# Kernel optimization log

Hardware: AMD Instinct MI355X
Metric: run time of the kernel (lower is better)

The kernel has to match this reference:

```python
import jax, jax.numpy as jnp
import numpy as np

H = 256      # hidden_dim
NH = 4       # num_heads (fixed in __init__)


def _mha_pool(x, mask, Wqkv, bqkv, Wo, bo):
    """Batched torch-style MultiheadAttention (self-attn) + masked mean pool.
    x: [..., L, H], mask: [..., L] float {0,1} (1 = valid).
    Returns pooled embedding [..., H]. Fully-masked rows yield zeros
    (numerator is 0, denominator is 1e-10), matching the torch branch.
    """
    h = x.shape[-1]
    dh = h // NH
    qkv = x @ Wqkv.T + bqkv                      # [..., L, 3H]
    q, k, v = jnp.split(qkv, 3, axis=-1)
    split = lambda t: t.reshape(t.shape[:-1] + (NH, dh))
    q, k, v = split(q), split(k), split(v)
    scale = 1.0 / jnp.sqrt(jnp.asarray(dh, x.dtype))
    scores = jnp.einsum('...qhd,...khd->...hqk', q, k) * scale
    # key_padding_mask: masked keys get large negative logit
    scores = scores + (1.0 - mask)[..., None, None, :] * jnp.asarray(-1e9, x.dtype)
    attn = jax.nn.softmax(scores, axis=-1)
    o = jnp.einsum('...hqk,...khd->...qhd', attn, v)
    o = o.reshape(o.shape[:-2] + (h,)) @ Wo.T + bo   # out_proj
    pooled = (o * mask[..., None]).sum(-2) / (mask.sum(-1, keepdims=True) + 1e-10)
    return pooled


def _mha_params(key):
    k1, k2 = jax.random.split(key)
    s = 1.0 / np.sqrt(H)
    Wqkv = jax.random.uniform(k1, (3 * H, H), jnp.float32, -s, s)
    bqkv = jnp.zeros((3 * H,), jnp.float32)
    Wo = jax.random.uniform(k2, (H, H), jnp.float32, -s, s)
    bo = jnp.zeros((H,), jnp.float32)
    return Wqkv, bqkv, Wo, bo


def setup_inputs() -> dict:
    key = jax.random.key(0)
    k0, k1, kw, ks, kc = jax.random.split(key, 5)
    B, SEC, SEN, W = 16, 8, 16, 64
    we = jax.random.normal(k0, (B, SEC, SEN, W, H), jnp.float32)
    am = jax.random.randint(k1, (B, SEC, SEN, W), 0, 2, jnp.int32)
    wW, wb, wO, wob = _mha_params(kw)
    sW, sb, sO, sob = _mha_params(ks)
    cW, cb, cO, cob = _mha_params(kc)
    return {
        'word_embeddings': we, 'attention_mask': am,
        'word_Wqkv': wW, 'word_bqkv': wb, 'word_Wo': wO, 'word_bo': wob,
        'sent_Wqkv': sW, 'sent_bqkv': sb, 'sent_Wo': sO, 'sent_bo': sob,
        'sect_Wqkv': cW, 'sect_bqkv': cb, 'sect_Wo': cO, 'sect_bo': cob,
    }


def reference(word_embeddings, attention_mask,
              word_Wqkv, word_bqkv, word_Wo, word_bo,
              sent_Wqkv, sent_bqkv, sent_Wo, sent_bo,
              sect_Wqkv, sect_bqkv, sect_Wo, sect_bo):
    wm = attention_mask.astype(word_embeddings.dtype)            # [B,Sec,Sen,W]
    # word level -> sentence embeddings [B,Sec,Sen,H]
    sent = _mha_pool(word_embeddings, wm, word_Wqkv, word_bqkv, word_Wo, word_bo)
    # sentence level -> section embeddings [B,Sec,H]
    sm = (wm.sum(-1) > 0).astype(word_embeddings.dtype)          # [B,Sec,Sen]
    sect = _mha_pool(sent, sm, sent_Wqkv, sent_bqkv, sent_Wo, sent_bo)
    # section level -> doc embeddings [B,H]
    cm = (wm.sum((-1, -2)) > 0).astype(word_embeddings.dtype)    # [B,Sec]
    doc = _mha_pool(sect, cm, sect_Wqkv, sect_bqkv, sect_Wo, sect_bo)
    return doc
```

## Files before the change

### kernel.cpp

```cpp
#include <hip/hip_runtime.h>
#include <hip/hip_bf16.h>


typedef short bf16x8 __attribute__((ext_vector_type(8)));
typedef float f32x4 __attribute__((ext_vector_type(4)));
typedef unsigned int u32x4 __attribute__((ext_vector_type(4)));
typedef unsigned short U16;
typedef unsigned int U32;

__device__ __forceinline__ U32 bf16_rne(float f) {
    U32 u = __builtin_bit_cast(U32, f);
    return (u + 0x7FFFu + ((u >> 16) & 1u)) >> 16;
}
__device__ __forceinline__ void split_hl(float f, U16& h, U16& l) {
    U32 hu = bf16_rne(f);
    float hf = __builtin_bit_cast(float, hu << 16);
    h = (U16)hu;
    l = (U16)bf16_rne(f - hf);
}
__device__ __forceinline__ U32 pack_hl(float f) {
    U32 hu = bf16_rne(f);
    float hf = __builtin_bit_cast(float, hu << 16);
    U32 lo = bf16_rne(f - hf);
    return (hu << 16) | (lo & 0xFFFFu);
}

__device__ __forceinline__ void unpack8(u32x4 a, u32x4 b, u32x4& hi, u32x4& lo) {
    hi[0] = __builtin_amdgcn_perm(a[1], a[0], 0x07060302u);
    hi[1] = __builtin_amdgcn_perm(a[3], a[2], 0x07060302u);
    hi[2] = __builtin_amdgcn_perm(b[1], b[0], 0x07060302u);
    hi[3] = __builtin_amdgcn_perm(b[3], b[2], 0x07060302u);
    lo[0] = __builtin_amdgcn_perm(a[1], a[0], 0x05040100u);
    lo[1] = __builtin_amdgcn_perm(a[3], a[2], 0x05040100u);
    lo[2] = __builtin_amdgcn_perm(b[1], b[0], 0x05040100u);
    lo[3] = __builtin_amdgcn_perm(b[3], b[2], 0x05040100u);
}

#define MFMA(A, B, C) __builtin_amdgcn_mfma_f32_16x16x32_bf16( \
    __builtin_bit_cast(bf16x8, A), __builtin_bit_cast(bf16x8, B), C, 0, 0, 0)

__device__ __forceinline__ void tile_frag(const U32* tile, int row, int s0,
                                          u32x4& hi, u32x4& lo) {
    int m = row & 15;
    u32x4 a = *(const u32x4*)(tile + row * 64 + ((s0    ) ^ m) * 4);
    u32x4 b = *(const u32x4*)(tile + row * 64 + ((s0 + 1) ^ m) * 4);
    unpack8(a, b, hi, lo);
}
__device__ __forceinline__ void tile_put(U32* tile, int row, int col, float v) {
    tile[row * 64 + (((col >> 2) ^ (row & 15))) * 4 + (col & 3)] = pack_hl(v);
}

template <int RS, int SW>
__device__ __forceinline__ u32x4 fragp(const U16* base, int row, int k, int lhi) {
    int slot = ((k >> 3) + lhi) ^ (row & SW);
    return *(const u32x4*)(base + row * RS + slot * 8);
}
template <int RS, int SW>
__device__ __forceinline__ void put16(U16* base, int row, int col, U16 v) {
    int slot = (col >> 3) ^ (row & SW);
    base[row * RS + slot * 8 + (col & 7)] = v;
}
template <int RS, int SW>
__device__ __forceinline__ void put64(U16* base, int row, int col0,
                                      U16 v0, U16 v1, U16 v2, U16 v3) {
    int slot = (col0 >> 3) ^ (row & SW);
    U32* p = (U32*)(base + row * RS + slot * 8 + (col0 & 7));
    p[0] = (U32)v0 | ((U32)v1 << 16);
    p[1] = (U32)v2 | ((U32)v3 << 16);
}

__global__ __launch_bounds__(256) void convert_w(
    const float* __restrict__ Wq, const float* __restrict__ Wo,
    U16* __restrict__ qh, U16* __restrict__ ql,
    U16* __restrict__ oh, U16* __restrict__ ol)
{
    int i = blockIdx.x * 256 + threadIdx.x;
    if (i < 768 * 256) { U16 h, l; split_hl(Wq[i], h, l); qh[i] = h; ql[i] = l; }
    if (i < 256 * 256) { U16 h, l; split_hl(Wo[i], h, l); oh[i] = h; ol[i] = l; }
}

__global__ __launch_bounds__(256, 2) void word_mfma(
    const float* __restrict__ x, const int* __restrict__ am,
    const U16* __restrict__ Wqh, const U16* __restrict__ Wql,
    const float* __restrict__ bqkv,
    const float* __restrict__ Wo32,
    const float* __restrict__ bo,
    U16* __restrict__ sent_hi, U16* __restrict__ sent_lo,
    float* __restrict__ smask)
{
    __shared__ __align__(16) U32 Qs[64 * 64];
    __shared__ __align__(16) U32 Ks[64 * 64];
    __shared__ __align__(16) U32 VX[64 * 64];
    __shared__ float msk[64];
    __shared__ float smsum;

    const int t = threadIdx.x;
    const int w = t >> 6, l = t & 63, l15 = l & 15, lhi = l >> 4;
    const int b = blockIdx.x;
    const float* xb = x + (size_t)b * 16384;

    if (t < 64) msk[t] = (float)am[b * 64 + t];

    const int r0 = t >> 3, c8 = t & 7;
    const int r1 = r0 + 32;
    const int mm0 = r0 & 15, mm1 = r1 & 15;

    float po[16];

    #pragma unroll 1
    for (int h = 0; h < 4; ++h) {
        float4 s00 = *(const float4*)(xb + r0 * 256 + c8 * 8);
        float4 s01 = *(const float4*)(xb + r0 * 256 + c8 * 8 + 4);
        float4 s10 = *(const float4*)(xb + r1 * 256 + c8 * 8);
        float4 s11 = *(const float4*)(xb + r1 * 256 + c8 * 8 + 4);
        f32x4 acc[3][4];
        #pragma unroll
        for (int j = 0; j < 3; ++j)
            #pragma unroll
            for (int mt = 0; mt < 4; ++mt) acc[j][mt] = f32x4{0.f, 0.f, 0.f, 0.f};

        for (int kc = 0; kc < 4; ++kc) {
            __syncthreads();
            {
                u32x4 p0, p1;
                p0[0] = pack_hl(s00.x); p0[1] = pack_hl(s00.y);
                p0[2] = pack_hl(s00.z); p0[3] = pack_hl(s00.w);
                p1[0] = pack_hl(s01.x); p1[1] = pack_hl(s01.y);
                p1[2] = pack_hl(s01.z); p1[3] = pack_hl(s01.w);
                *(u32x4*)(VX + r0 * 64 + ((c8 * 2    ) ^ mm0) * 4) = p0;
                *(u32x4*)(VX + r0 * 64 + ((c8 * 2 + 1) ^ mm0) * 4) = p1;
                p0[0] = pack_hl(s10.x); p0[1] = pack_hl(s10.y);
                p0[2] = pack_hl(s10.z); p0[3] = pack_hl(s10.w);
                p1[0] = pack_hl(s11.x); p1[1] = pack_hl(s11.y);
                p1[2] = pack_hl(s11.z); p1[3] = pack_hl(s11.w);
                *(u32x4*)(VX + r1 * 64 + ((c8 * 2    ) ^ mm1) * 4) = p0;
                *(u32x4*)(VX + r1 * 64 + ((c8 * 2 + 1) ^ mm1) * 4) = p1;
            }
            __syncthreads();
            if (kc < 3) {
                s00 = *(const float4*)(xb + r0 * 256 + (kc + 1) * 64 + c8 * 8);
                s01 = *(const float4*)(xb + r0 * 256 + (kc + 1) * 64 + c8 * 8 + 4);
                s10 = *(const float4*)(xb + r1 * 256 + (kc + 1) * 64 + c8 * 8);
                s11 = *(const float4*)(xb + r1 * 256 + (kc + 1) * 64 + c8 * 8 + 4);
            }
            #pragma unroll
            for (int ks = 0; ks < 2; ++ks) {
                const int s0 = ks * 8 + lhi * 2;
                const int kk = kc * 64 + ks * 32 + lhi * 8;
                const size_t wr0 = (size_t)(          h * 64 + w * 16 + l15) * 256 + kk;
                const size_t wr1 = (size_t)(256     + h * 64 + w * 16 + l15) * 256 + kk;
                const size_t wr2 = (size_t)(512     + h * 64 + w * 16 + l15) * 256 + kk;
                u32x4 wh0 = *(const u32x4*)(Wqh + wr0);
                u32x4 wl0 = *(const u32x4*)(Wql + wr0);
                u32x4 wh1 = *(const u32x4*)(Wqh + wr1);
                u32x4 wl1 = *(const u32x4*)(Wql + wr1);
                u32x4 wh2 = *(const u32x4*)(Wqh + wr2);
                u32x4 wl2 = *(const u32x4*)(Wql + wr2);
                #pragma unroll
                for (int mt = 0; mt < 4; ++mt) {
                    u32x4 xh, xl;
                    tile_frag(VX, mt * 16 + l15, s0, xh, xl);
                    acc[0][mt] = MFMA(xh, wh0, acc[0][mt]);
                    acc[0][mt] = MFMA(xh, wl0, acc[0][mt]);
                    acc[0][mt] = MFMA(xl, wh0, acc[0][mt]);
                    acc[1][mt] = MFMA(xh, wh1, acc[1][mt]);
                    acc[1][mt] = MFMA(xh, wl1, acc[1][mt]);
                    acc[1][mt] = MFMA(xl, wh1, acc[1][mt]);
                    acc[2][mt] = MFMA(xh, wh2, acc[2][mt]);
                    acc[2][mt] = MFMA(xh, wl2, acc[2][mt]);
                    acc[2][mt] = MFMA(xl, wh2, acc[2][mt]);
                }
            }
        }
        {
            const float bQ = bqkv[      h * 64 + w * 16 + l15];
            const float bK = bqkv[256 + h * 64 + w * 16 + l15];
            #pragma unroll
            for (int mt = 0; mt < 4; ++mt) {
                #pragma unroll
                for (int r = 0; r < 4; ++r) {
                    tile_put(Qs, mt * 16 + lhi * 4 + r, w * 16 + l15, acc[0][mt][r] + bQ);
                    tile_put(Ks, mt * 16 + lhi * 4 + r, w * 16 + l15, acc[1][mt][r] + bK);
                }
            }
        }
        __syncthreads();
        {
            const float bV = bqkv[512 + h * 64 + w * 16 + l15];
            const int d = w * 16 + l15;
            #pragma unroll
            for (int mt = 0; mt < 4; ++mt) {
                u32x4 pv;
                #pragma unroll
                for (int r = 0; r < 4; ++r) pv[r] = pack_hl(acc[2][mt][r] + bV);
                const int cs = (mt * 4 + lhi) ^ (d & 15);
                *(u32x4*)(VX + d * 64 + cs * 4) = pv;
            }
        }
        __syncthreads();
        if (h == 0 && t == 0) {
            float s = 0.f;
            for (int i = 0; i < 64; ++i) s += msk[i];
            smsum = s;
        }

        {
            f32x4 sa[4];
            #pragma unroll
            for (int i = 0; i < 4; ++i) sa[i] = f32x4{0.f, 0.f, 0.f, 0.f};
            #pragma unroll
            for (int ks = 0; ks < 2; ++ks) {
                const int s0 = ks * 8 + lhi * 2;
                u32x4 qh, ql;
                tile_frag(Qs, w * 16 + l15, s0, qh, ql);
                #pragma unroll
                for (int nt = 0; nt < 4; ++nt) {
                    u32x4 kh, kl;
                    tile_frag(Ks, nt * 16 + l15, s0, kh, kl);
                    sa[nt] = MFMA(qh, kh, sa[nt]);
                    sa[nt] = MFMA(qh, kl, sa[nt]);
                    sa[nt] = MFMA(ql, kh, sa[nt]);
                }
            }
            float sc[4][4];
            #pragma unroll
            for (int nt = 0; nt < 4; ++nt) {
                const float mterm = (1.0f - msk[nt * 16 + l15]) * -1e9f;
                #pragma unroll
                for (int r = 0; r < 4; ++r) sc[nt][r] = sa[nt][r] * 0.125f + mterm;
            }
            #pragma unroll
            for (int r = 0; r < 4; ++r) {
                float m = fmaxf(fmaxf(sc[0][r], sc[1][r]), fmaxf(sc[2][r], sc[3][r]));
                #pragma unroll
                for (int off = 1; off < 16; off <<= 1) m = fmaxf(m, __shfl_xor(m, off));
                float e0 = expf(sc[0][r] - m), e1 = expf(sc[1][r] - m);
                float e2 = expf(sc[2][r] - m), e3 = expf(sc[3][r] - m);
                float s = e0 + e1 + e2 + e3;
                #pragma unroll
                for (int off = 1; off < 16; off <<= 1) s += __shfl_xor(s, off);
                const float inv = 1.0f / s;
                sc[0][r] = e0 * inv; sc[1][r] = e1 * inv;
                sc[2][r] = e2 * inv; sc[3][r] = e3 * inv;
            }
            #pragma unroll
            for (int nt = 0; nt < 4; ++nt)
                #pragma unroll
                for (int r = 0; r < 4; ++r)
                    tile_put(Qs, w * 16 + lhi * 4 + r, nt * 16 + l15, sc[nt][r]);
        }
        {
            f32x4 pa[4];
            #pragma unroll
            for (int i = 0; i < 4; ++i) pa[i] = f32x4{0.f, 0.f, 0.f, 0.f};
            #pragma unroll
            for (int ks = 0; ks < 2; ++ks) {
                const int s0 = ks * 8 + lhi * 2;
                u32x4 ph, pl;
                tile_frag(Qs, w * 16 + l15, s0, ph, pl);
                #pragma unroll
                for (int nt = 0; nt < 4; ++nt) {
                    u32x4 vh, vl;
                    tile_frag(VX, nt * 16 + l15, s0, vh, vl);
                    pa[nt] = MFMA(ph, vh, pa[nt]);
                    pa[nt] = MFMA(ph, vl, pa[nt]);
                    pa[nt] = MFMA(pl, vh, pa[nt]);
                }
            }
            float sarr[4];
            #pragma unroll
            for (int nt = 0; nt < 4; ++nt) {
                float s = 0.f;
                #pragma unroll
                for (int r = 0; r < 4; ++r)
                    s += msk[w * 16 + lhi * 4 + r] * pa[nt][r];
                s += __shfl_xor(s, 16);
                s += __shfl_xor(s, 32);
                sarr[nt] = s;
            }
            if (h == 0) {
                po[0] = sarr[0]; po[1] = sarr[1]; po[2] = sarr[2]; po[3] = sarr[3];
            } else if (h == 1) {
                po[4] = sarr[0]; po[5] = sarr[1]; po[6] = sarr[2]; po[7] = sarr[3];
            } else if (h == 2) {
                po[8] = sarr[0]; po[9] = sarr[1]; po[10] = sarr[2]; po[11] = sarr[3];
            } else {
                po[12] = sarr[0]; po[13] = sarr[1]; po[14] = sarr[2]; po[15] = sarr[3];
            }
        }
    }

    __syncthreads();
    float (*part)[256] = (float(*)[256])Ks;
    if (lhi == 0) {
        #pragma unroll
        for (int hh = 0; hh < 4; ++hh)
            #pragma unroll
            for (int nt = 0; nt < 4; ++nt)
                part[w][hh * 64 + nt * 16 + l15] = po[hh * 4 + nt];
    }
    __syncthreads();
    {
        float opv = part[0][t] + part[1][t] + part[2][t] + part[3][t];
        part[0][t] = opv;
    }
    __syncthreads();
    {
        const float* wrow = Wo32 + (size_t)t * 256;
        const float* opool = part[0];
        float s = 0.f;
        #pragma unroll 8
        for (int c = 0; c < 256; c += 4) {
            float4 wv = *(const float4*)(wrow + c);
            s += opool[c] * wv.x + opool[c + 1] * wv.y
               + opool[c + 2] * wv.z + opool[c + 3] * wv.w;
        }
        float m = smsum;
        float val = (s + bo[t] * m) / (m + 1e-10f);
        U16 vH, vL; split_hl(val, vH, vL);
        sent_hi[(size_t)b * 256 + t] = vH;
        sent_lo[(size_t)b * 256 + t] = vL;
    }
    if (t == 0) smask[b] = (smsum > 0.f) ? 1.f : 0.f;
}

template <int L>
__global__ __launch_bounds__(256) void mha_small(
    const U16* __restrict__ xh, const U16* __restrict__ xl,
    const float* __restrict__ mk,
    const U16* __restrict__ Wqh, const U16* __restrict__ Wql,
    const float* __restrict__ bqkv,
    const U16* __restrict__ Woh, const U16* __restrict__ Wol,
    const float* __restrict__ bo,
    float* __restrict__ out_f32, U16* __restrict__ out_hi, U16* __restrict__ out_lo,
    float* __restrict__ outmask)
{
    __shared__ __align__(16) U16 xs_h[16*256], xs_l[16*256];
    __shared__ __align__(16) U16 Qh_[16*256], Ql_[16*256];
    __shared__ __align__(16) U16 Kh_[16*256], Kl_[16*256];
    __shared__ __align__(16) U16 Vh_[256*32], Vl_[256*32];
    __shared__ __align__(16) U16 Ph_[4][16*32], Pl_[4][16*32];
    __shared__ __align__(16) U16 Oh_[16*256], Ol_[16*256];
    __shared__ float msk[16];
    __shared__ float smsum;

    const int t = threadIdx.x;
    const int w = t >> 6, l = t & 63, l15 = l & 15, lhi = l >> 4;
    const int b = blockIdx.x;

    if (t < 16) msk[t] = (t < L) ? mk[b*L + t] : 0.f;

    #pragma unroll
    for (int i = 0; i < 2; ++i) {
        int c = i*256 + t;
        int row = c >> 5, c8 = c & 31;
        u32x4 hv = u32x4{0,0,0,0}, lv = u32x4{0,0,0,0};
        if (row < L) {
            hv = *(const u32x4*)(xh + ((size_t)b*L + row)*256 + c8*8);
            lv = *(const u32x4*)(xl + ((size_t)b*L + row)*256 + c8*8);
        }
        int slot = c8 ^ (row & 7);
        *(u32x4*)(xs_h + row*256 + slot*8) = hv;
        *(u32x4*)(xs_l + row*256 + slot*8) = lv;
    }
    #pragma unroll
    for (int i = 0; i < 4; ++i) {
        int c = i*256 + t;
        *(u32x4*)(Vh_ + c*8) = u32x4{0,0,0,0};
        *(u32x4*)(Vl_ + c*8) = u32x4{0,0,0,0};
    }
    *(u32x4*)(&Ph_[0][0] + t*8) = u32x4{0,0,0,0};
    *(u32x4*)(&Pl_[0][0] + t*8) = u32x4{0,0,0,0};
    __syncthreads();
    if (t == 0) { float s = 0.f; for (int i = 0; i < 16; ++i) s += msk[i]; smsum = s; }

    {
        f32x4 acc[12];
        #pragma unroll
        for (int i = 0; i < 12; ++i) acc[i] = f32x4{0.f,0.f,0.f,0.f};
        #pragma unroll 2
        for (int k0 = 0; k0 < 256; k0 += 32) {
            u32x4 ah = fragp<256,7>(xs_h, l15, k0, lhi);
            u32x4 al = fragp<256,7>(xs_l, l15, k0, lhi);
            #pragma unroll
            for (int j = 0; j < 12; ++j) {
                int u = w*12 + j;
                u32x4 wh = *(const u32x4*)(Wqh + (size_t)(u*16 + l15)*256 + k0 + lhi*8);
                u32x4 wl = *(const u32x4*)(Wql + (size_t)(u*16 + l15)*256 + k0 + lhi*8);
                acc[j] = MFMA(ah, wh, acc[j]);
                acc[j] = MFMA(ah, wl, acc[j]);
                acc[j] = MFMA(al, wh, acc[j]);
            }
        }
        #pragma unroll
        for (int j = 0; j < 12; ++j) {
            int u = w*12 + j;
            int mat = u >> 4, cg = u & 15;
            float bias = bqkv[u*16 + l15];
            if (mat < 2) {
                U16* dh = (mat == 0) ? Qh_ : Kh_;
                U16* dl = (mat == 0) ? Ql_ : Kl_;
                #pragma unroll
                for (int r = 0; r < 4; ++r) {
                    U16 vH, vL; split_hl(acc[j][r] + bias, vH, vL);
                    put16<256,7>(dh, lhi*4 + r, cg*16 + l15, vH);
                    put16<256,7>(dl, lhi*4 + r, cg*16 + l15, vL);
                }
            } else {
                U16 h4[4], l4[4];
                #pragma unroll
                for (int r = 0; r < 4; ++r) split_hl(acc[j][r] + bias, h4[r], l4[r]);
                put64<32,3>(Vh_, cg*16 + l15, lhi*4, h4[0],h4[1],h4[2],h4[3]);
                put64<32,3>(Vl_, cg*16 + l15, lhi*4, l4[0],l4[1],l4[2],l4[3]);
            }
        }
    }
    __syncthreads();

    {
        const int h = w;
        f32x4 sa = f32x4{0.f,0.f,0.f,0.f};
        #pragma unroll
        for (int k0 = 0; k0 < 64; k0 += 32) {
            u32x4 qh = fragp<256,7>(Qh_, l15, h*64 + k0, lhi);
            u32x4 ql = fragp<256,7>(Ql_, l15, h*64 + k0, lhi);
            u32x4 kh = fragp<256,7>(Kh_, l15, h*64 + k0, lhi);
            u32x4 kl = fragp<256,7>(Kl_, l15, h*64 + k0, lhi);
            sa = MFMA(qh, kh, sa);
            sa = MFMA(qh, kl, sa);
            sa = MFMA(ql, kh, sa);
        }
        float sc[4];
        float mterm = (1.0f - msk[l15]) * -1e9f;
        #pragma unroll
        for (int r = 0; r < 4; ++r) sc[r] = sa[r] * 0.125f + mterm;
        #pragma unroll
        for (int r = 0; r < 4; ++r) {
            float m = sc[r];
            #pragma unroll
            for (int off = 1; off < 16; off <<= 1) m = fmaxf(m, __shfl_xor(m, off));
            float e = expf(sc[r] - m);
            float s = e;
            #pragma unroll
            for (int off = 1; off < 16; off <<= 1) s += __shfl_xor(s, off);
            sc[r] = e / s;
        }
        #pragma unroll
        for (int r = 0; r < 4; ++r) {
            U16 vH, vL; split_hl(sc[r], vH, vL);
            put16<32,3>(&Ph_[h][0], lhi*4 + r, l15, vH);
            put16<32,3>(&Pl_[h][0], lhi*4 + r, l15, vL);
        }
        f32x4 pa[4];
        #pragma unroll
        for (int i = 0; i < 4; ++i) pa[i] = f32x4{0.f,0.f,0.f,0.f};
        {
            u32x4 ph = fragp<32,3>(&Ph_[h][0], l15, 0, lhi);
            u32x4 pl = fragp<32,3>(&Pl_[h][0], l15, 0, lhi);
            #pragma unroll
            for (int ntl = 0; ntl < 4; ++ntl) {
                u32x4 vh = fragp<32,3>(Vh_, h*64 + ntl*16 + l15, 0, lhi);
                u32x4 vl = fragp<32,3>(Vl_, h*64 + ntl*16 + l15, 0, lhi);
                pa[ntl] = MFMA(ph, vh, pa[ntl]);
                pa[ntl] = MFMA(ph, vl, pa[ntl]);
                pa[ntl] = MFMA(pl, vh, pa[ntl]);
            }
        }
        #pragma unroll
        for (int ntl = 0; ntl < 4; ++ntl) {
            #pragma unroll
            for (int r = 0; r < 4; ++r) {
                U16 vH, vL; split_hl(pa[ntl][r], vH, vL);
                put16<256,7>(Oh_, lhi*4 + r, h*64 + ntl*16 + l15, vH);
                put16<256,7>(Ol_, lhi*4 + r, h*64 + ntl*16 + l15, vL);
            }
        }
    }
    __syncthreads();

    {
        f32x4 acc4[4];
        #pragma unroll
        for (int i = 0; i < 4; ++i) acc4[i] = f32x4{0.f,0.f,0.f,0.f};
        #pragma unroll 2
        for (int k0 = 0; k0 < 256; k0 += 32) {
            u32x4 oh = fragp<256,7>(Oh_, l15, k0, lhi);
            u32x4 ol = fragp<256,7>(Ol_, l15, k0, lhi);
            #pragma unroll
            for (int j = 0; j < 4; ++j) {
                int oc = w*64 + j*16 + l15;
                u32x4 wh = *(const u32x4*)(Woh + (size_t)oc*256 + k0 + lhi*8);
                u32x4 wl = *(const u32x4*)(Wol + (size_t)oc*256 + k0 + lhi*8);
                acc4[j] = MFMA(oh, wh, acc4[j]);
                acc4[j] = MFMA(oh, wl, acc4[j]);
                acc4[j] = MFMA(ol, wh, acc4[j]);
            }
        }
        float msum = smsum;
        #pragma unroll
        for (int j = 0; j < 4; ++j) {
            float s = 0.f;
            #pragma unroll
            for (int r = 0; r < 4; ++r) s += msk[lhi*4 + r] * acc4[j][r];
            s += __shfl_xor(s, 16);
            s += __shfl_xor(s, 32);
            if (lhi == 0) {
                int col = w*64 + j*16 + l15;
                float val = (s + bo[col] * msum) / (msum + 1e-10f);
                if (out_f32) out_f32[(size_t)b*256 + col] = val;
                if (out_hi) {
                    U16 vH, vL; split_hl(val, vH, vL);
                    out_hi[(size_t)b*256 + col] = vH;
                    out_lo[(size_t)b*256 + col] = vL;
                }
            }
        }
    }
    if (t == 0 && outmask) outmask[b] = (smsum > 0.f) ? 1.f : 0.f;
}

extern "C" void kernel_launch(void* const* d_in, const int* in_sizes, int n_in,
                              void* d_out, int out_size, void* d_ws, size_t ws_size,
                              hipStream_t stream) {
    (void)in_sizes; (void)n_in; (void)out_size; (void)ws_size;
    const float* we  = (const float*)d_in[0];
    const int*   am  = (const int*)d_in[1];
    const float* wW  = (const float*)d_in[2];
    const float* wb  = (const float*)d_in[3];
    const float* wO  = (const float*)d_in[4];
    const float* wob = (const float*)d_in[5];
    const float* sW  = (const float*)d_in[6];
    const float* sb  = (const float*)d_in[7];
    const float* sO  = (const float*)d_in[8];
    const float* sob = (const float*)d_in[9];
    const float* cW  = (const float*)d_in[10];
    const float* cb  = (const float*)d_in[11];
    const float* cO  = (const float*)d_in[12];
    const float* cob = (const float*)d_in[13];

    U16* p = (U16*)d_ws;
    U16* sent_hi = p; p += 2048*256;
    U16* sent_lo = p; p += 2048*256;
    U16* sect_hi = p; p += 128*256;
    U16* sect_lo = p; p += 128*256;
    U16* w1qh = p; p += 768*256;  U16* w1ql = p; p += 768*256;
    U16* w1oh = p; p += 256*256;  U16* w1ol = p; p += 256*256;
    U16* w2qh = p; p += 768*256;  U16* w2ql = p; p += 768*256;
    U16* w2oh = p; p += 256*256;  U16* w2ol = p; p += 256*256;
    U16* w3qh = p; p += 768*256;  U16* w3ql = p; p += 768*256;
    U16* w3oh = p; p += 256*256;  U16* w3ol = p; p += 256*256;
    float* smaskb = (float*)p;
    float* cmaskb = smaskb + 2048;

    convert_w<<<768, 256, 0, stream>>>(wW, wO, w1qh, w1ql, w1oh, w1ol);
    convert_w<<<768, 256, 0, stream>>>(sW, sO, w2qh, w2ql, w2oh, w2ol);
    convert_w<<<768, 256, 0, stream>>>(cW, cO, w3qh, w3ql, w3oh, w3ol);
    word_mfma<<<2048, 256, 0, stream>>>(we, am, w1qh, w1ql, wb, wO, wob,
                                        sent_hi, sent_lo, smaskb);
    mha_small<16><<<128, 256, 0, stream>>>(sent_hi, sent_lo, smaskb,
                                           w2qh, w2ql, sb, w2oh, w2ol, sob,
                                           nullptr, sect_hi, sect_lo, cmaskb);
    mha_small<8><<<16, 256, 0, stream>>>(sect_hi, sect_lo, cmaskb,
                                         w3qh, w3ql, cb, w3oh, w3ol, cob,
                                         (float*)d_out, nullptr, nullptr, nullptr);
}
```

Baseline: 438.7 us.

## Raise word kernel occupancy, drop register prefetch, use intrinsic bf16 conversion

Raises the word_mfma launch bounds from 2 to 3 blocks per SU and removes the software prefetch of the next x chunk held in registers, loading each chunk just before it is converted. The manual bf16 round-to-nearest-even bit trick is replaced with the HIP __float2bfloat16 intrinsic. The intent is to cut register pressure so more waves can hide latency, at the cost of losing explicit global-load overlap with the MFMA loop. The intrinsic may also lower to fewer instructions.

```diff
diff --git a/kernel.cpp b/kernel.cpp
--- a/kernel.cpp
+++ b/kernel.cpp
@@ -8,21 +8,20 @@
 typedef unsigned short U16;
 typedef unsigned int U32;
 
-__device__ __forceinline__ U32 bf16_rne(float f) {
-    U32 u = __builtin_bit_cast(U32, f);
-    return (u + 0x7FFFu + ((u >> 16) & 1u)) >> 16;
+__device__ __forceinline__ U16 f2bf(float f) {
+    __hip_bfloat16 b = __float2bfloat16(f);
+    return __builtin_bit_cast(U16, b);
 }
 __device__ __forceinline__ void split_hl(float f, U16& h, U16& l) {
-    U32 hu = bf16_rne(f);
-    float hf = __builtin_bit_cast(float, hu << 16);
-    h = (U16)hu;
-    l = (U16)bf16_rne(f - hf);
+    h = f2bf(f);
+    float hf = __builtin_bit_cast(float, (U32)h << 16);
+    l = f2bf(f - hf);
 }
 __device__ __forceinline__ U32 pack_hl(float f) {
-    U32 hu = bf16_rne(f);
-    float hf = __builtin_bit_cast(float, hu << 16);
-    U32 lo = bf16_rne(f - hf);
-    return (hu << 16) | (lo & 0xFFFFu);
+    U32 h = f2bf(f);
+    float hf = __builtin_bit_cast(float, h << 16);
+    U32 lo = f2bf(f - hf);
+    return (h << 16) | lo;
 }
 
 __device__ __forceinline__ void unpack8(u32x4 a, u32x4 b, u32x4& hi, u32x4& lo) {
@@ -79,7 +78,7 @@
     if (i < 256 * 256) { U16 h, l; split_hl(Wo[i], h, l); oh[i] = h; ol[i] = l; }
 }
 
-__global__ __launch_bounds__(256, 2) void word_mfma(
+__global__ __launch_bounds__(256, 3) void word_mfma(
     const float* __restrict__ x, const int* __restrict__ am,
     const U16* __restrict__ Wqh, const U16* __restrict__ Wql,
     const float* __restrict__ bqkv,
@@ -109,10 +108,6 @@
 
     #pragma unroll 1
     for (int h = 0; h < 4; ++h) {
-        float4 s00 = *(const float4*)(xb + r0 * 256 + c8 * 8);
-        float4 s01 = *(const float4*)(xb + r0 * 256 + c8 * 8 + 4);
-        float4 s10 = *(const float4*)(xb + r1 * 256 + c8 * 8);
-        float4 s11 = *(const float4*)(xb + r1 * 256 + c8 * 8 + 4);
         f32x4 acc[3][4];
         #pragma unroll
         for (int j = 0; j < 3; ++j)
@@ -122,6 +117,10 @@
         for (int kc = 0; kc < 4; ++kc) {
             __syncthreads();
             {
+                float4 s00 = *(const float4*)(xb + r0 * 256 + kc * 64 + c8 * 8);
+                float4 s01 = *(const float4*)(xb + r0 * 256 + kc * 64 + c8 * 8 + 4);
+                float4 s10 = *(const float4*)(xb + r1 * 256 + kc * 64 + c8 * 8);
+                float4 s11 = *(const float4*)(xb + r1 * 256 + kc * 64 + c8 * 8 + 4);
                 u32x4 p0, p1;
                 p0[0] = pack_hl(s00.x); p0[1] = pack_hl(s00.y);
                 p0[2] = pack_hl(s00.z); p0[3] = pack_hl(s00.w);
@@ -137,12 +136,6 @@
                 *(u32x4*)(VX + r1 * 64 + ((c8 * 2 + 1) ^ mm1) * 4) = p1;
             }
             __syncthreads();
-            if (kc < 3) {
-                s00 = *(const float4*)(xb + r0 * 256 + (kc + 1) * 64 + c8 * 8);
-                s01 = *(const float4*)(xb + r0 * 256 + (kc + 1) * 64 + c8 * 8 + 4);
-                s10 = *(const float4*)(xb + r1 * 256 + (kc + 1) * 64 + c8 * 8);
-                s11 = *(const float4*)(xb + r1 * 256 + (kc + 1) * 64 + c8 * 8 + 4);
-            }
             #pragma unroll
             for (int ks = 0; ks < 2; ++ks) {
                 const int s0 = ks * 8 + lhi * 2;
```

Result: slower. 447.5 us (+2.0%).
